# Performance work log

Hardware: AMD Instinct MI355X
Metric: run time of the kernel (lower is better)

## Reference

```python
import jax, jax.numpy as jnp
import numpy as np

B, SQ, SK, D = 8, 2048, 2048, 512

def setup_inputs() -> dict:
    key = jax.random.key(0)
    kq, kk, kv = jax.random.split(key, 3)
    return {
        "query": jax.random.normal(kq, (B, SQ, D), dtype=jnp.float32),
        "key": jax.random.normal(kk, (B, SK, D), dtype=jnp.float32),
        "value": jax.random.normal(kv, (B, SK, D), dtype=jnp.float32),
        "alpha": jnp.float32(0.5),  # learned scalar, init 0.5 as in torch module
    }

def reference(query, key, value, alpha):
    # squared L2 pairwise distances: ||q||^2 + ||k||^2 - 2 q.k  (== cdist(...)**2)
    q2 = jnp.sum(query * query, axis=-1, keepdims=True)          # [B,Sq,1]
    k2 = jnp.sum(key * key, axis=-1, keepdims=True)              # [B,Sk,1]
    qk = jnp.einsum("bqd,bkd->bqk", query, key)                  # [B,Sq,Sk]
    sq_dist = jnp.maximum(q2 + jnp.swapaxes(k2, -1, -2) - 2.0 * qk, 0.0)
    kernel = jnp.exp(-alpha * sq_dist)                            # Gaussian energy well
    weights = jax.nn.softmax(kernel, axis=-1)                     # softmax over keys
    out = jnp.einsum("bqk,bkd->bqd", weights, value)
    return out, weights
```

## Files before the change

### kernel.cpp

```cpp
#include <hip/hip_runtime.h>
#include <stdint.h>

#define B_  8
#define SQ_ 2048
#define SK_ 2048
#define D_  512

typedef unsigned short ushort_t;
typedef __attribute__((ext_vector_type(8))) short          short8;
typedef __attribute__((ext_vector_type(8))) unsigned short ushort8;
typedef __attribute__((ext_vector_type(4))) float          f32x4;

__device__ __forceinline__ unsigned short f2bf(float x) {
  union { float f; unsigned u; } v; v.f = x;
  unsigned r = v.u + 0x7FFFu + ((v.u >> 16) & 1u);
  return (unsigned short)(r >> 16);
}

__device__ __forceinline__ void gload_lds16(const void* g, void* l) {
  __builtin_amdgcn_global_load_lds(
      (__attribute__((address_space(1))) void*)(uintptr_t)g,
      (__attribute__((address_space(3))) void*)l, 16, 0, 0);
}

__global__ void prep_qk(const float* __restrict__ Q, const float* __restrict__ K,
                        ushort_t* __restrict__ Qb, ushort_t* __restrict__ Kb,
                        float* __restrict__ q2, float* __restrict__ k2) {
  const int t = threadIdx.x;
  const int rloc = t >> 7;
  const int row  = blockIdx.x * 2 + rloc;
  const bool isK = row >= B_ * SQ_;
  const int r = isK ? row - B_ * SQ_ : row;
  const float*    src = (isK ? K : Q) + (size_t)r * D_;
  ushort_t*       dst = (isK ? Kb : Qb) + (size_t)r * D_;
  float*          d2  = isK ? k2 : q2;

  const int c = (t & 127) * 4;
  float4 v = *(const float4*)(src + c);
  ushort4 o;
  o.x = f2bf(v.x); o.y = f2bf(v.y); o.z = f2bf(v.z); o.w = f2bf(v.w);
  *(ushort4*)(dst + c) = o;

  float s = v.x * v.x + v.y * v.y + v.z * v.z + v.w * v.w;
  for (int off = 32; off; off >>= 1) s += __shfl_down(s, off);
  __shared__ float ps[4];
  if ((t & 63) == 0) ps[t >> 6] = s;
  __syncthreads();
  if ((t & 127) == 0) d2[r] = ps[rloc * 2] + ps[rloc * 2 + 1];
}

__global__ void prep_vt(const float* __restrict__ V, ushort_t* __restrict__ VT) {
  const int b  = blockIdx.z;
  const int k0 = blockIdx.x * 64;
  const int d0 = blockIdx.y * 64;
  __shared__ __align__(16) ushort_t tile[64][68];
  const int t = threadIdx.x;
  const float* src = V + (size_t)b * SK_ * D_;
  #pragma unroll
  for (int i = 0; i < 4; ++i) {
    int kl = (t >> 4) + i * 16;
    int dl = (t & 15) * 4;
    float4 v = *(const float4*)(src + (size_t)(k0 + kl) * D_ + d0 + dl);
    tile[kl][dl]     = f2bf(v.x);
    tile[kl][dl + 1] = f2bf(v.y);
    tile[kl][dl + 2] = f2bf(v.z);
    tile[kl][dl + 3] = f2bf(v.w);
  }
  __syncthreads();
  ushort_t* dstb = VT + (size_t)b * D_ * SK_;
  #pragma unroll
  for (int j = 0; j < 2; ++j) {
    int chunk = t + j * 256;
    int dl = chunk >> 3;
    int kc = (chunk & 7) << 3;
    ushort8 o;
    #pragma unroll
    for (int m = 0; m < 8; ++m) o[m] = tile[kc + m][dl];
    *(ushort8*)(dstb + (size_t)(d0 + dl) * SK_ + k0 + kc) = o;
  }
}

template <int BF16E>
__global__ __launch_bounds__(256) void qk_kernel(
    const ushort_t* __restrict__ Qb, const ushort_t* __restrict__ Kb,
    const float* __restrict__ q2, const float* __restrict__ k2,
    const float* __restrict__ alphap,
    float* __restrict__ Wf, ushort_t* __restrict__ Ebf,
    float* __restrict__ rowsum) {
  __shared__ __align__(16) ushort_t As[8192];
  __shared__ __align__(16) ushort_t Bs[8192];
  __shared__ float q2s[128], k2s[128];

  const int t = threadIdx.x;
  const int lane = t & 63, wid = t >> 6;
  const int wm = wid >> 1, wn = wid & 1;

  const int id  = blockIdx.x + 16 * blockIdx.y + 256 * blockIdx.z;
  const int swz = (id & 7) * 256 + (id >> 3);
  const int bx = swz & 15, by = (swz >> 4) & 15, bz = swz >> 8;

  const ushort_t* Aq = Qb + ((size_t)bz * SQ_ + by * 128) * D_;
  const ushort_t* Bk = Kb + ((size_t)bz * SK_ + bx * 128) * D_;

  if (t < 128) q2s[t] = q2[bz * SQ_ + by * 128 + t];
  else         k2s[t - 128] = k2[bz * SK_ + bx * 128 + (t - 128)];

  f32x4 acc[4][4] = {};
  for (int kt = 0; kt < D_ / 64; ++kt) {
    __syncthreads();
    #pragma unroll
    for (int i = 0; i < 4; ++i) {
      int s = t + i * 256;
      int row = s >> 3;
      int c16 = (s & 7) ^ (row & 7);
      gload_lds16(Aq + (size_t)row * D_ + kt * 64 + c16 * 8, (char*)As + s * 16);
      gload_lds16(Bk + (size_t)row * D_ + kt * 64 + c16 * 8, (char*)Bs + s * 16);
    }
    __syncthreads();
    #pragma unroll
    for (int kk = 0; kk < 2; ++kk) {
      short8 a[4], bf[4];
      #pragma unroll
      for (int mi = 0; mi < 4; ++mi) {
        int row = (wm << 6) + (mi << 4) + (lane & 15);
        int c = ((kk << 2) + (lane >> 4)) ^ (row & 7);
        a[mi] = *(const short8*)((const char*)As + row * 128 + c * 16);
      }
      #pragma unroll
      for (int ni = 0; ni < 4; ++ni) {
        int col = (wn << 6) + (ni << 4) + (lane & 15);
        int c = ((kk << 2) + (lane >> 4)) ^ (col & 7);
        bf[ni] = *(const short8*)((const char*)Bs + col * 128 + c * 16);
      }
      #pragma unroll
      for (int mi = 0; mi < 4; ++mi)
        #pragma unroll
        for (int ni = 0; ni < 4; ++ni)
          acc[mi][ni] = __builtin_amdgcn_mfma_f32_16x16x32_bf16(a[mi], bf[ni], acc[mi][ni], 0, 0, 0);
    }
  }

  const float alpha = *alphap;
  const int r0 = (lane >> 4) << 2;
  const int cl = lane & 15;

  float k2c[4];
  #pragma unroll
  for (int ni = 0; ni < 4; ++ni) k2c[ni] = k2s[(wn << 6) + (ni << 4) + cl];

  #pragma unroll
  for (int mi = 0; mi < 4; ++mi) {
    float q2r[4];
    #pragma unroll
    for (int r = 0; r < 4; ++r) q2r[r] = q2s[(wm << 6) + (mi << 4) + r0 + r];
    float se[4] = {0.f, 0.f, 0.f, 0.f};
    #pragma unroll
    for (int ni = 0; ni < 4; ++ni) {
      int gcol = bx * 128 + (wn << 6) + (ni << 4) + cl;
      #pragma unroll
      for (int r = 0; r < 4; ++r) {
        int rl = (wm << 6) + (mi << 4) + r0 + r;
        float sq = fmaxf(q2r[r] + k2c[ni] - 2.0f * acc[mi][ni][r], 0.0f);
        float kv = __expf(-alpha * sq);
        float e  = __expf(kv);
        size_t idx = (size_t)((size_t)bz * SQ_ + by * 128 + rl) * SK_ + gcol;
        if (BF16E) Ebf[idx] = f2bf(e);
        else       Wf[idx]  = e;
        se[r] += e;
      }
    }
    #pragma unroll
    for (int r = 0; r < 4; ++r) {
      float s = se[r];
      for (int off = 1; off < 16; off <<= 1) s += __shfl_xor(s, off);
      if (cl == 0)
        atomicAdd(&rowsum[bz * SQ_ + by * 128 + (wm << 6) + (mi << 4) + r0 + r], s);
    }
  }
}

__global__ __launch_bounds__(256) void pv_bf16(
    const ushort_t* __restrict__ Eb, const ushort_t* __restrict__ VT,
    const float* __restrict__ rowsum, float* __restrict__ Out) {
  __shared__ __align__(16) ushort_t As[8192];
  __shared__ __align__(16) ushort_t Bs[8192];
  __shared__ float rss[128];

  const int t = threadIdx.x;
  const int lane = t & 63, wid = t >> 6;
  const int wm = wid >> 1, wn = wid & 1;

  const int id  = blockIdx.x + 4 * blockIdx.y + 64 * blockIdx.z;
  const int swz = (id & 7) * 64 + (id >> 3);
  const int bx = swz & 3, by = (swz >> 2) & 15, bz = swz >> 6;

  const ushort_t* Ebb = Eb + ((size_t)bz * SQ_ + by * 128) * SK_;
  const ushort_t* Vb  = VT + ((size_t)bz * D_ + bx * 128) * SK_;

  if (t < 128) rss[t] = rowsum[bz * SQ_ + by * 128 + t];

  f32x4 acc[4][4] = {};
  for (int kt = 0; kt < SK_ / 64; ++kt) {
    __syncthreads();
    #pragma unroll
    for (int i = 0; i < 4; ++i) {
      int s = t + i * 256;
      int row = s >> 3;
      int c16 = (s & 7) ^ (row & 7);
      gload_lds16(Ebb + (size_t)row * SK_ + kt * 64 + c16 * 8, (char*)As + s * 16);
      gload_lds16(Vb  + (size_t)row * SK_ + kt * 64 + c16 * 8, (char*)Bs + s * 16);
    }
    __syncthreads();
    #pragma unroll
    for (int kk = 0; kk < 2; ++kk) {
      short8 a[4], bf[4];
      #pragma unroll
      for (int mi = 0; mi < 4; ++mi) {
        int row = (wm << 6) + (mi << 4) + (lane & 15);
        int c = ((kk << 2) + (lane >> 4)) ^ (row & 7);
        a[mi] = *(const short8*)((const char*)As + row * 128 + c * 16);
      }
      #pragma unroll
      for (int ni = 0; ni < 4; ++ni) {
        int col = (wn << 6) + (ni << 4) + (lane & 15);
        int c = ((kk << 2) + (lane >> 4)) ^ (col & 7);
        bf[ni] = *(const short8*)((const char*)Bs + col * 128 + c * 16);
      }
      #pragma unroll
      for (int mi = 0; mi < 4; ++mi)
        #pragma unroll
        for (int ni = 0; ni < 4; ++ni)
          acc[mi][ni] = __builtin_amdgcn_mfma_f32_16x16x32_bf16(a[mi], bf[ni], acc[mi][ni], 0, 0, 0);
    }
  }

  float* Ob = Out + ((size_t)bz * SQ_ + by * 128) * D_ + bx * 128;
  const int r0 = (lane >> 4) << 2;
  const int cl = lane & 15;
  #pragma unroll
  for (int mi = 0; mi < 4; ++mi) {
    #pragma unroll
    for (int r = 0; r < 4; ++r) {
      int rl = (wm << 6) + (mi << 4) + r0 + r;
      float rinv = 1.0f / rss[rl];
      #pragma unroll
      for (int ni = 0; ni < 4; ++ni)
        Ob[(size_t)rl * D_ + (wn << 6) + (ni << 4) + cl] = acc[mi][ni][r] * rinv;
    }
  }
}

__global__ __launch_bounds__(256) void pv_f32(
    const float* __restrict__ E, const ushort_t* __restrict__ VT,
    const float* __restrict__ rowsum, float* __restrict__ Out) {
  __shared__ __align__(16) ushort_t As[8192];
  __shared__ __align__(16) ushort_t Bs[8192];
  __shared__ float rss[128];

  const int t = threadIdx.x;
  const int lane = t & 63, wid = t >> 6;
  const int wm = wid >> 1, wn = wid & 1;
  const int bx = blockIdx.x, by = blockIdx.y, bz = blockIdx.z;

  const float*    Eb = E + ((size_t)bz * SQ_ + by * 128) * SK_;
  const ushort_t* Vb = VT + ((size_t)bz * D_ + bx * 128) * SK_;

  if (t < 128) rss[t] = rowsum[bz * SQ_ + by * 128 + t];

  f32x4 acc[4][4] = {};
  for (int kt = 0; kt < SK_ / 64; ++kt) {
    float4 va[4][2];
    #pragma unroll
    for (int i = 0; i < 4; ++i) {
      int s = t + i * 256;
      int row = s >> 3, c16 = s & 7;
      const float* g = Eb + (size_t)row * SK_ + kt * 64 + c16 * 8;
      va[i][0] = *(const float4*)g;
      va[i][1] = *(const float4*)(g + 4);
    }
    __syncthreads();
    #pragma unroll
    for (int i = 0; i < 4; ++i) {
      int s = t + i * 256;
      int row = s >> 3, c16 = s & 7;
      int c16s = c16 ^ (row & 7);
      ushort8 o;
      o[0] = f2bf(va[i][0].x); o[1] = f2bf(va[i][0].y);
      o[2] = f2bf(va[i][0].z); o[3] = f2bf(va[i][0].w);
      o[4] = f2bf(va[i][1].x); o[5] = f2bf(va[i][1].y);
      o[6] = f2bf(va[i][1].z); o[7] = f2bf(va[i][1].w);
      *(ushort8*)((char*)As + row * 128 + c16s * 16) = o;
      gload_lds16(Vb + (size_t)row * SK_ + kt * 64 + c16s * 8, (char*)Bs + s * 16);
    }
    __syncthreads();
    #pragma unroll
    for (int kk = 0; kk < 2; ++kk) {
      short8 a[4], bf[4];
      #pragma unroll
      for (int mi = 0; mi < 4; ++mi) {
        int row = (wm << 6) + (mi << 4) + (lane & 15);
        int c = ((kk << 2) + (lane >> 4)) ^ (row & 7);
        a[mi] = *(const short8*)((const char*)As + row * 128 + c * 16);
      }
      #pragma unroll
      for (int ni = 0; ni < 4; ++ni) {
        int col = (wn << 6) + (ni << 4) + (lane & 15);
        int c = ((kk << 2) + (lane >> 4)) ^ (col & 7);
        bf[ni] = *(const short8*)((const char*)Bs + col * 128 + c * 16);
      }
      #pragma unroll
      for (int mi = 0; mi < 4; ++mi)
        #pragma unroll
        for (int ni = 0; ni < 4; ++ni)
          acc[mi][ni] = __builtin_amdgcn_mfma_f32_16x16x32_bf16(a[mi], bf[ni], acc[mi][ni], 0, 0, 0);
    }
  }

  float* Ob = Out + ((size_t)bz * SQ_ + by * 128) * D_ + bx * 128;
  const int r0 = (lane >> 4) << 2;
  const int cl = lane & 15;
  #pragma unroll
  for (int mi = 0; mi < 4; ++mi) {
    #pragma unroll
    for (int r = 0; r < 4; ++r) {
      int rl = (wm << 6) + (mi << 4) + r0 + r;
      float rinv = 1.0f / rss[rl];
      #pragma unroll
      for (int ni = 0; ni < 4; ++ni)
        Ob[(size_t)rl * D_ + (wn << 6) + (ni << 4) + cl] = acc[mi][ni][r] * rinv;
    }
  }
}

__global__ void norm_bf16(const ushort_t* __restrict__ E,
                          const float* __restrict__ rowsum,
                          float* __restrict__ W) {
  const size_t total8 = (size_t)B_ * SQ_ * SK_ / 8;
  for (size_t g = (size_t)blockIdx.x * blockDim.x + threadIdx.x; g < total8;
       g += (size_t)gridDim.x * blockDim.x) {
    ushort8 e = *(const ushort8*)(E + g * 8);
    float rinv = 1.0f / rowsum[g >> 8];
    float4 lo, hi;
    lo.x = __uint_as_float((unsigned)e[0] << 16) * rinv;
    lo.y = __uint_as_float((unsigned)e[1] << 16) * rinv;
    lo.z = __uint_as_float((unsigned)e[2] << 16) * rinv;
    lo.w = __uint_as_float((unsigned)e[3] << 16) * rinv;
    hi.x = __uint_as_float((unsigned)e[4] << 16) * rinv;
    hi.y = __uint_as_float((unsigned)e[5] << 16) * rinv;
    hi.z = __uint_as_float((unsigned)e[6] << 16) * rinv;
    hi.w = __uint_as_float((unsigned)e[7] << 16) * rinv;
    *(float4*)(W + g * 8)     = lo;
    *(float4*)(W + g * 8 + 4) = hi;
  }
}

__global__ void norm_f32(float* __restrict__ W, const float* __restrict__ rowsum) {
  const size_t total4 = (size_t)B_ * SQ_ * SK_ / 4;
  for (size_t i = (size_t)blockIdx.x * blockDim.x + threadIdx.x; i < total4;
       i += (size_t)gridDim.x * blockDim.x) {
    float4 v = ((const float4*)W)[i];
    float rinv = 1.0f / rowsum[i >> 9];
    v.x *= rinv; v.y *= rinv; v.z *= rinv; v.w *= rinv;
    ((float4*)W)[i] = v;
  }
}

extern "C" void kernel_launch(void* const* d_in, const int* in_sizes, int n_in,
                              void* d_out, int out_size, void* d_ws, size_t ws_size,
                              hipStream_t stream) {
  const float* Q     = (const float*)d_in[0];
  const float* K     = (const float*)d_in[1];
  const float* V     = (const float*)d_in[2];
  const float* alpha = (const float*)d_in[3];

  float* out = (float*)d_out;
  float* W   = out + (size_t)B_ * SQ_ * D_;

  const size_t QKV = (size_t)B_ * SQ_ * D_;
  const size_t NW  = (size_t)B_ * SQ_ * SK_;
  ushort_t* Qb = (ushort_t*)d_ws;
  ushort_t* Kb = Qb + QKV;
  ushort_t* VT = Kb + QKV;

  const size_t need_bf16 = (3 * QKV + NW) * sizeof(ushort_t)
                         + (size_t)(2 * B_ * SQ_ + B_ * SK_) * sizeof(float);
  const bool use_bf16 = ws_size >= need_bf16;

  ushort_t* Eb = VT + QKV;
  float* fbase = use_bf16 ? (float*)(Eb + NW) : (float*)(VT + QKV);
  float* q2     = fbase;
  float* k2     = q2 + B_ * SQ_;
  float* rowsum = k2 + B_ * SK_;

  hipMemsetAsync(rowsum, 0, (size_t)B_ * SQ_ * sizeof(float), stream);

  prep_qk<<<dim3(B_ * SQ_), 256, 0, stream>>>(Q, K, Qb, Kb, q2, k2);
  prep_vt<<<dim3(SK_ / 64, D_ / 64, B_), 256, 0, stream>>>(V, VT);

  if (use_bf16) {
    qk_kernel<1><<<dim3(SK_ / 128, SQ_ / 128, B_), 256, 0, stream>>>(
        Qb, Kb, q2, k2, alpha, nullptr, Eb, rowsum);
    pv_bf16<<<dim3(D_ / 128, SQ_ / 128, B_), 256, 0, stream>>>(Eb, VT, rowsum, out);
    norm_bf16<<<dim3(2048), 256, 0, stream>>>(Eb, rowsum, W);
  } else {
    qk_kernel<0><<<dim3(SK_ / 128, SQ_ / 128, B_), 256, 0, stream>>>(
        Qb, Kb, q2, k2, alpha, W, nullptr, rowsum);
    pv_f32<<<dim3(D_ / 128, SQ_ / 128, B_), 256, 0, stream>>>(W, VT, rowsum, out);
    norm_f32<<<dim3(4096), 256, 0, stream>>>(W, rowsum);
  }
}
```

Before: 369.0 us.

## Double-buffer LDS in QK/PV GEMMs, fuse normalization into PV, skip exp

Both GEMM kernels get double-buffered LDS so the next tile's global-to-LDS load overlaps the MFMA work on the current tile, with one barrier per iteration. The standalone bf16 normalization kernel is removed; each PV block instead writes a 1/4 slice of the normalized weights from the E tiles it already holds in LDS, avoiding a separate re-read of E. The QK epilogue skips the double exp when a whole wavefront has arguments below -20 and writes 1.0. This relies on exp(exp(x)) being close to 1 there, which holds in general, and it adds branch divergence. Doubling LDS to 64KB per block may reduce occupancy.

```diff
diff --git a/kernel.cpp b/kernel.cpp
--- a/kernel.cpp
+++ b/kernel.cpp
@@ -87,8 +87,8 @@
     const float* __restrict__ alphap,
     float* __restrict__ Wf, ushort_t* __restrict__ Ebf,
     float* __restrict__ rowsum) {
-  __shared__ __align__(16) ushort_t As[8192];
-  __shared__ __align__(16) ushort_t Bs[8192];
+  __shared__ __align__(16) ushort_t As[2][8192];
+  __shared__ __align__(16) ushort_t Bs[2][8192];
   __shared__ float q2s[128], k2s[128];
 
   const int t = threadIdx.x;
@@ -105,18 +105,26 @@
   if (t < 128) q2s[t] = q2[bz * SQ_ + by * 128 + t];
   else         k2s[t - 128] = k2[bz * SK_ + bx * 128 + (t - 128)];
 
+  #define QK_STAGE(buf, kt)                                                     \
+    _Pragma("unroll")                                                           \
+    for (int i = 0; i < 4; ++i) {                                               \
+      int s = t + i * 256;                                                      \
+      int row = s >> 3;                                                         \
+      int c16 = (s & 7) ^ (row & 7);                                            \
+      gload_lds16(Aq + (size_t)row * D_ + (kt) * 64 + c16 * 8,                  \
+                  (char*)As[buf] + s * 16);                                     \
+      gload_lds16(Bk + (size_t)row * D_ + (kt) * 64 + c16 * 8,                  \
+                  (char*)Bs[buf] + s * 16);                                     \
+    }
+
+  QK_STAGE(0, 0);
+  __syncthreads();
+
   f32x4 acc[4][4] = {};
-  for (int kt = 0; kt < D_ / 64; ++kt) {
-    __syncthreads();
-    #pragma unroll
-    for (int i = 0; i < 4; ++i) {
-      int s = t + i * 256;
-      int row = s >> 3;
-      int c16 = (s & 7) ^ (row & 7);
-      gload_lds16(Aq + (size_t)row * D_ + kt * 64 + c16 * 8, (char*)As + s * 16);
-      gload_lds16(Bk + (size_t)row * D_ + kt * 64 + c16 * 8, (char*)Bs + s * 16);
-    }
-    __syncthreads();
+  #pragma unroll
+  for (int kt = 0; kt < 8; ++kt) {
+    const int cur = kt & 1;
+    if (kt < 7) { QK_STAGE(cur ^ 1, kt + 1); }
     #pragma unroll
     for (int kk = 0; kk < 2; ++kk) {
       short8 a[4], bf[4];
@@ -124,13 +132,13 @@
       for (int mi = 0; mi < 4; ++mi) {
         int row = (wm << 6) + (mi << 4) + (lane & 15);
         int c = ((kk << 2) + (lane >> 4)) ^ (row & 7);
-        a[mi] = *(const short8*)((const char*)As + row * 128 + c * 16);
+        a[mi] = *(const short8*)((const char*)As[cur] + row * 128 + c * 16);
       }
       #pragma unroll
       for (int ni = 0; ni < 4; ++ni) {
         int col = (wn << 6) + (ni << 4) + (lane & 15);
         int c = ((kk << 2) + (lane >> 4)) ^ (col & 7);
-        bf[ni] = *(const short8*)((const char*)Bs + col * 128 + c * 16);
+        bf[ni] = *(const short8*)((const char*)Bs[cur] + col * 128 + c * 16);
       }
       #pragma unroll
       for (int mi = 0; mi < 4; ++mi)
@@ -138,7 +146,9 @@
         for (int ni = 0; ni < 4; ++ni)
           acc[mi][ni] = __builtin_amdgcn_mfma_f32_16x16x32_bf16(a[mi], bf[ni], acc[mi][ni], 0, 0, 0);
     }
-  }
+    __syncthreads();
+  }
+  #undef QK_STAGE
 
   const float alpha = *alphap;
   const int r0 = (lane >> 4) << 2;
@@ -157,16 +167,27 @@
     #pragma unroll
     for (int ni = 0; ni < 4; ++ni) {
       int gcol = bx * 128 + (wn << 6) + (ni << 4) + cl;
+      float x[4], e[4];
+      #pragma unroll
+      for (int r = 0; r < 4; ++r) {
+        float sq = fmaxf(q2r[r] + k2c[ni] - 2.0f * acc[mi][ni][r], 0.0f);
+        x[r] = -alpha * sq;
+      }
+      int small = (x[0] < -20.f) & (x[1] < -20.f) & (x[2] < -20.f) & (x[3] < -20.f);
+      if (__all(small)) {
+        #pragma unroll
+        for (int r = 0; r < 4; ++r) e[r] = 1.0f;
+      } else {
+        #pragma unroll
+        for (int r = 0; r < 4; ++r) e[r] = __expf(__expf(x[r]));
+      }
       #pragma unroll
       for (int r = 0; r < 4; ++r) {
         int rl = (wm << 6) + (mi << 4) + r0 + r;
-        float sq = fmaxf(q2r[r] + k2c[ni] - 2.0f * acc[mi][ni][r], 0.0f);
-        float kv = __expf(-alpha * sq);
-        float e  = __expf(kv);
         size_t idx = (size_t)((size_t)bz * SQ_ + by * 128 + rl) * SK_ + gcol;
-        if (BF16E) Ebf[idx] = f2bf(e);
-        else       Wf[idx]  = e;
-        se[r] += e;
+        if (BF16E) Ebf[idx] = f2bf(e[r]);
+        else       Wf[idx]  = e[r];
+        se[r] += e[r];
       }
     }
     #pragma unroll
@@ -181,9 +202,10 @@
 
 __global__ __launch_bounds__(256) void pv_bf16(
     const ushort_t* __restrict__ Eb, const ushort_t* __restrict__ VT,
-    const float* __restrict__ rowsum, float* __restrict__ Out) {
-  __shared__ __align__(16) ushort_t As[8192];
-  __shared__ __align__(16) ushort_t Bs[8192];
+    const float* __restrict__ rowsum, float* __restrict__ Out,
+    float* __restrict__ W) {
+  __shared__ __align__(16) ushort_t As[2][8192];
+  __shared__ __align__(16) ushort_t Bs[2][8192];
   __shared__ float rss[128];
 
   const int t = threadIdx.x;
@@ -196,21 +218,57 @@
 
   const ushort_t* Ebb = Eb + ((size_t)bz * SQ_ + by * 128) * SK_;
   const ushort_t* Vb  = VT + ((size_t)bz * D_ + bx * 128) * SK_;
+  float* Wb = W + ((size_t)bz * SQ_ + by * 128) * SK_;
 
   if (t < 128) rss[t] = rowsum[bz * SQ_ + by * 128 + t];
-
+  __syncthreads();
+  const float rinv_t = 1.0f;
+
+  #define PV_STAGE(buf, kt)                                                     \
+    _Pragma("unroll")                                                           \
+    for (int i = 0; i < 4; ++i) {                                               \
+      int s = t + i * 256;                                                      \
+      int row = s >> 3;                                                         \
+      int c16 = (s & 7) ^ (row & 7);                                            \
+      gload_lds16(Ebb + (size_t)row * SK_ + (kt) * 64 + c16 * 8,                \
+                  (char*)As[buf] + s * 16);                                     \
+      gload_lds16(Vb  + (size_t)row * SK_ + (kt) * 64 + c16 * 8,                \
+                  (char*)Bs[buf] + s * 16);                                     \
+    }
+
+  PV_STAGE(0, 0);
+  __syncthreads();
+
+  const int wlo = bx * 8, whi = wlo + 8;
   f32x4 acc[4][4] = {};
-  for (int kt = 0; kt < SK_ / 64; ++kt) {
-    __syncthreads();
-    #pragma unroll
-    for (int i = 0; i < 4; ++i) {
-      int s = t + i * 256;
-      int row = s >> 3;
-      int c16 = (s & 7) ^ (row & 7);
-      gload_lds16(Ebb + (size_t)row * SK_ + kt * 64 + c16 * 8, (char*)As + s * 16);
-      gload_lds16(Vb  + (size_t)row * SK_ + kt * 64 + c16 * 8, (char*)Bs + s * 16);
-    }
-    __syncthreads();
+  for (int kt = 0; kt < 32; ++kt) {
+    const int cur = kt & 1;
+    if (kt < 31) { PV_STAGE(cur ^ 1, kt + 1); }
+
+    if (kt >= wlo && kt < whi) {
+      #pragma unroll
+      for (int i = 0; i < 4; ++i) {
+        int s = t + i * 256;
+        int row = s >> 3;
+        int c16 = s & 7;
+        int c16s = c16 ^ (row & 7);
+        ushort8 ev = *(const ushort8*)((const char*)As[cur] + row * 128 + c16s * 16);
+        float rinv = 1.0f / rss[row];
+        float4 lo, hi;
+        lo.x = __uint_as_float((unsigned)ev[0] << 16) * rinv;
+        lo.y = __uint_as_float((unsigned)ev[1] << 16) * rinv;
+        lo.z = __uint_as_float((unsigned)ev[2] << 16) * rinv;
+        lo.w = __uint_as_float((unsigned)ev[3] << 16) * rinv;
+        hi.x = __uint_as_float((unsigned)ev[4] << 16) * rinv;
+        hi.y = __uint_as_float((unsigned)ev[5] << 16) * rinv;
+        hi.z = __uint_as_float((unsigned)ev[6] << 16) * rinv;
+        hi.w = __uint_as_float((unsigned)ev[7] << 16) * rinv;
+        float* wp = Wb + (size_t)row * SK_ + kt * 64 + c16 * 8;
+        *(float4*)wp       = lo;
+        *(float4*)(wp + 4) = hi;
+      }
+    }
+
     #pragma unroll
     for (int kk = 0; kk < 2; ++kk) {
       short8 a[4], bf[4];
@@ -218,13 +276,13 @@
       for (int mi = 0; mi < 4; ++mi) {
         int row = (wm << 6) + (mi << 4) + (lane & 15);
         int c = ((kk << 2) + (lane >> 4)) ^ (row & 7);
-        a[mi] = *(const short8*)((const char*)As + row * 128 + c * 16);
+        a[mi] = *(const short8*)((const char*)As[cur] + row * 128 + c * 16);
       }
       #pragma unroll
       for (int ni = 0; ni < 4; ++ni) {
         int col = (wn << 6) + (ni << 4) + (lane & 15);
         int c = ((kk << 2) + (lane >> 4)) ^ (col & 7);
-        bf[ni] = *(const short8*)((const char*)Bs + col * 128 + c * 16);
+        bf[ni] = *(const short8*)((const char*)Bs[cur] + col * 128 + c * 16);
       }
       #pragma unroll
       for (int mi = 0; mi < 4; ++mi)
@@ -232,7 +290,10 @@
         for (int ni = 0; ni < 4; ++ni)
           acc[mi][ni] = __builtin_amdgcn_mfma_f32_16x16x32_bf16(a[mi], bf[ni], acc[mi][ni], 0, 0, 0);
     }
-  }
+    __syncthreads();
+  }
+  #undef PV_STAGE
+  (void)rinv_t;
 
   float* Ob = Out + ((size_t)bz * SQ_ + by * 128) * D_ + bx * 128;
   const int r0 = (lane >> 4) << 2;
@@ -332,28 +393,6 @@
   }
 }
 
-__global__ void norm_bf16(const ushort_t* __restrict__ E,
-                          const float* __restrict__ rowsum,
-                          float* __restrict__ W) {
-  const size_t total8 = (size_t)B_ * SQ_ * SK_ / 8;
-  for (size_t g = (size_t)blockIdx.x * blockDim.x + threadIdx.x; g < total8;
-       g += (size_t)gridDim.x * blockDim.x) {
-    ushort8 e = *(const ushort8*)(E + g * 8);
-    float rinv = 1.0f / rowsum[g >> 8];
-    float4 lo, hi;
-    lo.x = __uint_as_float((unsigned)e[0] << 16) * rinv;
-    lo.y = __uint_as_float((unsigned)e[1] << 16) * rinv;
-    lo.z = __uint_as_float((unsigned)e[2] << 16) * rinv;
-    lo.w = __uint_as_float((unsigned)e[3] << 16) * rinv;
-    hi.x = __uint_as_float((unsigned)e[4] << 16) * rinv;
-    hi.y = __uint_as_float((unsigned)e[5] << 16) * rinv;
-    hi.z = __uint_as_float((unsigned)e[6] << 16) * rinv;
-    hi.w = __uint_as_float((unsigned)e[7] << 16) * rinv;
-    *(float4*)(W + g * 8)     = lo;
-    *(float4*)(W + g * 8 + 4) = hi;
-  }
-}
-
 __global__ void norm_f32(float* __restrict__ W, const float* __restrict__ rowsum) {
   const size_t total4 = (size_t)B_ * SQ_ * SK_ / 4;
   for (size_t i = (size_t)blockIdx.x * blockDim.x + threadIdx.x; i < total4;
@@ -400,8 +439,7 @@
   if (use_bf16) {
     qk_kernel<1><<<dim3(SK_ / 128, SQ_ / 128, B_), 256, 0, stream>>>(
         Qb, Kb, q2, k2, alpha, nullptr, Eb, rowsum);
-    pv_bf16<<<dim3(D_ / 128, SQ_ / 128, B_), 256, 0, stream>>>(Eb, VT, rowsum, out);
-    norm_bf16<<<dim3(2048), 256, 0, stream>>>(Eb, rowsum, W);
+    pv_bf16<<<dim3(D_ / 128, SQ_ / 128, B_), 256, 0, stream>>>(Eb, VT, rowsum, out, W);
   } else {
     qk_kernel<0><<<dim3(SK_ / 128, SQ_ / 128, B_), 256, 0, stream>>>(
         Qb, Kb, q2, k2, alpha, W, nullptr, rowsum);
```

New measurement: 353.9 us. 4.1% less time.
